# Performance work log

Measured on AMD Instinct MI355X. Metric: run time of the kernel, lower is better.

The kernel has to match this reference:

```python
import jax, jax.numpy as jnp
import numpy as np

EMBED_DIM = 1024
NUM_HEADS = 16
HEAD_DIM = EMBED_DIM // NUM_HEADS
WL_CHANNELS = 16
BATCH = 1
SEQ = 1024
KERR = 2.7e-18 * 1e6  # kerr_coefficient * 1e6 -> phase = KERR * |x|^2
SCALE = 1.0 / np.sqrt(HEAD_DIM)
W_INIT = 0.02


def setup_inputs() -> dict:
    key = jax.random.key(0)
    ks = jax.random.split(key, 7)
    x = jax.random.normal(ks[0], (BATCH, SEQ, EMBED_DIM), dtype=jnp.float32)
    Wq = jax.random.normal(ks[1], (EMBED_DIM, EMBED_DIM), dtype=jnp.float32) * W_INIT
    Wk = jax.random.normal(ks[2], (EMBED_DIM, EMBED_DIM), dtype=jnp.float32) * W_INIT
    Wv = jax.random.normal(ks[3], (EMBED_DIM, EMBED_DIM), dtype=jnp.float32) * W_INIT
    Wo = jax.random.normal(ks[4], (EMBED_DIM, EMBED_DIM), dtype=jnp.float32) * W_INIT
    bq = jnp.zeros((EMBED_DIM,), jnp.float32)
    bk = jnp.zeros((EMBED_DIM,), jnp.float32)
    bv = jnp.zeros((EMBED_DIM,), jnp.float32)
    bo = jnp.zeros((EMBED_DIM,), jnp.float32)
    phase_modulators = jax.random.normal(ks[5], (WL_CHANNELS, NUM_HEADS), dtype=jnp.float32)
    interference_weights = jnp.ones((WL_CHANNELS,), jnp.float32)
    return {"x": x, "Wq": Wq, "bq": bq, "Wk": Wk, "bk": bk, "Wv": Wv, "bv": bv,
            "Wo": Wo, "bo": bo, "phase_modulators": phase_modulators,
            "interference_weights": interference_weights}


def reference(x, Wq, bq, Wk, bk, Wv, bv, Wo, bo, phase_modulators, interference_weights):
    B, S, E = x.shape
    H, D = NUM_HEADS, HEAD_DIM

    def proj(W, b):
        # [B,S,E] -> [B,H,S,D]
        y = jnp.einsum('bse,ef->bsf', x, W) + b
        return y.reshape(B, S, H, D).transpose(0, 2, 1, 3)

    Q = proj(Wq, bq)
    K = proj(Wk, bk)
    V = proj(Wv, bv)

    # exp(1j*phase).real == cos(phase) for real phase
    cos_pm = jnp.cos(phase_modulators)  # [W, H]

    def wl_step(acc, wl):
        cpm, iw = wl  # cpm: [H], iw: scalar
        m = cpm[None, :, None, None]
        Qw = Q * m
        Kw = K * m
        scores = jnp.einsum('bhqd,bhkd->bhqk', Qw, Kw) * SCALE
        # Kerr nonlinearity: x * cos(KERR * x^2)
        scores = scores * jnp.cos(KERR * scores * scores)
        attn = jax.nn.softmax(scores, axis=-1)
        out = jnp.einsum('bhqk,bhkd->bhqd', attn, V)
        return acc + out * iw, None

    acc0 = jnp.zeros((B, H, S, D), x.dtype)
    acc, _ = jax.lax.scan(wl_step, acc0, (cos_pm, interference_weights))
    combined = acc / WL_CHANNELS  # mean over wavelength channels
    combined = combined.transpose(0, 2, 1, 3).reshape(B, S, E)
    return jnp.einsum('bse,ef->bsf', combined, Wo) + bo
```

## Files before the change

### kernel.cpp

```cpp
#include <hip/hip_runtime.h>
#include <hip/hip_fp16.h>
#include <math.h>

#define NH 16
#define NWL 16
#define NPOLY 10

typedef _Float16 half8 __attribute__((ext_vector_type(8)));
typedef _Float16 half4 __attribute__((ext_vector_type(4)));
typedef float f32x4 __attribute__((ext_vector_type(4)));

__global__ __launch_bounds__(256)
void cast_x_k(const float* __restrict__ X, _Float16* __restrict__ Xh)
{
    const int i = (blockIdx.x * 256 + threadIdx.x) * 8;
    float4 v0 = *(const float4*)&X[i];
    float4 v1 = *(const float4*)&X[i + 4];
    half8 o;
    o[0] = (_Float16)v0.x; o[1] = (_Float16)v0.y; o[2] = (_Float16)v0.z; o[3] = (_Float16)v0.w;
    o[4] = (_Float16)v1.x; o[5] = (_Float16)v1.y; o[6] = (_Float16)v1.z; o[7] = (_Float16)v1.w;
    *(half8*)&Xh[i] = o;
}

__global__ __launch_bounds__(256)
void castT_w(const float* __restrict__ W0, const float* __restrict__ W1,
             const float* __restrict__ W2, const float* __restrict__ W3,
             _Float16* __restrict__ WT)
{
    const float* W = W0;
    if (blockIdx.z == 1) W = W1;
    if (blockIdx.z == 2) W = W2;
    if (blockIdx.z == 3) W = W3;
    _Float16* out = WT + ((size_t)blockIdx.z << 20);

    __shared__ float Ts[64][65];
    const int t = threadIdx.x;
    const int ebase = blockIdx.y * 64;
    const int fbase = blockIdx.x * 64;

    {
        const int r0 = (t >> 4) * 4;
        const int c0 = (t & 15) * 4;
#pragma unroll
        for (int r = 0; r < 4; ++r) {
            float4 v = *(const float4*)&W[(size_t)(ebase + r0 + r) * 1024 + fbase + c0];
            Ts[r0 + r][c0 + 0] = v.x;
            Ts[r0 + r][c0 + 1] = v.y;
            Ts[r0 + r][c0 + 2] = v.z;
            Ts[r0 + r][c0 + 3] = v.w;
        }
    }
    __syncthreads();

    const int f = t >> 2;
    const int eseg = (t & 3) * 16;
    half8 lo, hi;
#pragma unroll
    for (int j = 0; j < 8; ++j) lo[j] = (_Float16)Ts[eseg + j][f];
#pragma unroll
    for (int j = 0; j < 8; ++j) hi[j] = (_Float16)Ts[eseg + 8 + j][f];
    *(half8*)&out[(size_t)(fbase + f) * 1024 + ebase + eseg]     = lo;
    *(half8*)&out[(size_t)(fbase + f) * 1024 + ebase + eseg + 8] = hi;
}

template<int MODE>
__global__ __launch_bounds__(256)
void gemm_mfma(const _Float16* __restrict__ A,
               const _Float16* __restrict__ BtBase,
               const float* __restrict__ B0, const float* __restrict__ B1,
               const float* __restrict__ B2,
               void* __restrict__ O0p, void* __restrict__ O1p, void* __restrict__ O2p)
{
    const int z = blockIdx.z;
    const _Float16* Bt = BtBase + ((size_t)z << 20);
    const float* bias = B0; void* Op = O0p;
    if (z == 1) { bias = B1; Op = O1p; }
    if (z == 2) { bias = B2; Op = O2p; }

    __shared__ _Float16 As[2][64][40];
    __shared__ _Float16 Bs[2][64][40];

    const int t = threadIdx.x;
    const int lane = t & 63;
    const int w = t >> 6;
    const int w_r = w >> 1;
    const int w_c = w & 1;
    const int sbase = blockIdx.y * 64;
    const int fbase = blockIdx.x * 64;

    const int srow = t >> 2;
    const int skseg = (t & 3) * 8;

    f32x4 acc[2][2];
#pragma unroll
    for (int m = 0; m < 2; ++m)
#pragma unroll
        for (int n = 0; n < 2; ++n) acc[m][n] = (f32x4){0.f, 0.f, 0.f, 0.f};

    const int lr = lane & 15;
    const int lk = (lane >> 4) * 8;

    {
        *(half8*)&As[0][srow][skseg] = *(const half8*)&A [(size_t)(sbase + srow) * 1024 + skseg];
        *(half8*)&Bs[0][srow][skseg] = *(const half8*)&Bt[(size_t)(fbase + srow) * 1024 + skseg];
    }
    __syncthreads();

    for (int tile = 0; tile < 32; ++tile) {
        const int cur = tile & 1;
        if (tile < 31) {
            const int kb = (tile + 1) * 32;
            half8 av = *(const half8*)&A [(size_t)(sbase + srow) * 1024 + kb + skseg];
            half8 bv = *(const half8*)&Bt[(size_t)(fbase + srow) * 1024 + kb + skseg];
            *(half8*)&As[cur ^ 1][srow][skseg] = av;
            *(half8*)&Bs[cur ^ 1][srow][skseg] = bv;
        }
        half8 a0 = *(const half8*)&As[cur][w_r * 32 + 0  + lr][lk];
        half8 a1 = *(const half8*)&As[cur][w_r * 32 + 16 + lr][lk];
        half8 b0 = *(const half8*)&Bs[cur][w_c * 32 + 0  + lr][lk];
        half8 b1 = *(const half8*)&Bs[cur][w_c * 32 + 16 + lr][lk];
        acc[0][0] = __builtin_amdgcn_mfma_f32_16x16x32_f16(a0, b0, acc[0][0], 0, 0, 0);
        acc[0][1] = __builtin_amdgcn_mfma_f32_16x16x32_f16(a0, b1, acc[0][1], 0, 0, 0);
        acc[1][0] = __builtin_amdgcn_mfma_f32_16x16x32_f16(a1, b0, acc[1][0], 0, 0, 0);
        acc[1][1] = __builtin_amdgcn_mfma_f32_16x16x32_f16(a1, b1, acc[1][1], 0, 0, 0);
        __syncthreads();
    }

#pragma unroll
    for (int m = 0; m < 2; ++m) {
        const int row0 = sbase + w_r * 32 + m * 16 + (lane >> 4) * 4;
#pragma unroll
        for (int n = 0; n < 2; ++n) {
            const int col = fbase + w_c * 32 + n * 16 + (lane & 15);
            const float bval = bias[col];
            if (MODE == 0) {
                float* O = (float*)Op;
#pragma unroll
                for (int r = 0; r < 4; ++r)
                    O[(size_t)(row0 + r) * 1024 + col] = acc[m][n][r] + bval;
            } else {
                _Float16* O = (_Float16*)Op;
                const int hh = col >> 6;
                const int d = col & 63;
                if (z == 2) {
                    half4 o;
#pragma unroll
                    for (int r = 0; r < 4; ++r) o[r] = (_Float16)(acc[m][n][r] + bval);
                    *(half4*)&O[((size_t)hh << 16) + (size_t)d * 1024 + row0] = o;
                } else {
#pragma unroll
                    for (int r = 0; r < 4; ++r)
                        O[((size_t)hh << 16) + (size_t)(row0 + r) * 64 + d] =
                            (_Float16)(acc[m][n][r] + bval);
                }
            }
        }
    }
}

__global__ __launch_bounds__(256, 4)
void attn_k(const _Float16* __restrict__ Qg, const _Float16* __restrict__ Kg,
            const _Float16* __restrict__ Vg, const float* __restrict__ pm,
            const float* __restrict__ iwp, _Float16* __restrict__ comb)
{
    const int wg  = blockIdx.x;
    const int xcd = wg & 7;
    const int idx = wg >> 3;
    const int h   = xcd * 2 + (idx >> 6);
    const int qt  = idx & 63;

    const int t = threadIdx.x;
    const int lane = t & 63;
    const int w = t >> 6;
    const int lr = lane & 15;
    const int lg = lane >> 4;

    __shared__ float Sred[4][16][68];
    __shared__ _Float16 Ps[4][16][72];
    __shared__ float sa[16], siw[16];
    __shared__ float gt[16][NPOLY + 1];

    if (t < 16) {
        float m = cosf(pm[t * NH + h]);
        sa[t] = m * m * 0.125f * 1.44269504f;
        siw[t] = iwp[t];
    }
    __syncthreads();

    float amin = sa[0], amax = sa[0];
#pragma unroll
    for (int i = 1; i < NWL; ++i) {
        amin = fminf(amin, sa[i]);
        amax = fmaxf(amax, sa[i]);
    }
    const float abar = 0.5f * (amin + amax);

    if (t < 16) {
        float g = (sa[t] - abar) * 0.69314718f;
        float p = 1.f;
        gt[t][0] = 1.f;
#pragma unroll
        for (int n = 1; n <= NPOLY; ++n) {
            p *= g / (float)n;
            gt[t][n] = p;
        }
    }

    const _Float16* Qrow = Qg + ((size_t)h << 16) + (size_t)(qt * 16 + lr) * 64;
    half8 q0 = *(const half8*)&Qrow[lg * 8];
    half8 q1 = *(const half8*)&Qrow[32 + lg * 8];
    __syncthreads();

    const _Float16* Kq = Kg + ((size_t)h << 16) + (size_t)w * 256 * 64;
    const _Float16* Vh = Vg + ((size_t)h << 16);

    float M[NPOLY + 1];
#pragma unroll
    for (int n = 0; n <= NPOLY; ++n) M[n] = 0.f;

    for (int ch = 0; ch < 4; ++ch) {
#pragma unroll
        for (int kf = 0; kf < 4; ++kf) {
            const _Float16* Kr = Kq + (size_t)(ch * 64 + kf * 16 + lr) * 64;
            half8 a0 = *(const half8*)&Kr[lg * 8];
            half8 a1 = *(const half8*)&Kr[32 + lg * 8];
            f32x4 s2 = (f32x4){0.f, 0.f, 0.f, 0.f};
            s2 = __builtin_amdgcn_mfma_f32_16x16x32_f16(a0, q0, s2, 0, 0, 0);
            s2 = __builtin_amdgcn_mfma_f32_16x16x32_f16(a1, q1, s2, 0, 0, 0);
#pragma unroll
            for (int r = 0; r < 4; ++r) {
                const float sv = s2[r];
                float e = exp2f(abar * sv);
                M[0] += e;
#pragma unroll
                for (int n = 1; n <= NPOLY; ++n) {
                    e *= sv;
                    M[n] += e;
                }
            }
        }
    }

#pragma unroll
    for (int off = 16; off < 64; off <<= 1)
#pragma unroll
        for (int n = 0; n <= NPOLY; ++n)
            M[n] += __shfl_xor(M[n], off);

    if (lg == 0) {
#pragma unroll
        for (int n = 0; n <= NPOLY; ++n) Sred[w][lr][n] = M[n];
    }
    __syncthreads();

#pragma unroll
    for (int n = 0; n <= NPOLY; ++n)
        M[n] = Sred[0][lr][n] + Sred[1][lr][n] + Sred[2][lr][n] + Sred[3][lr][n];

    float c[NPOLY + 1];
#pragma unroll
    for (int n = 0; n <= NPOLY; ++n) c[n] = 0.f;
#pragma unroll
    for (int i = 0; i < NWL; ++i) {
        float den = 0.f;
#pragma unroll
        for (int n = 0; n <= NPOLY; ++n) den = fmaf(gt[i][n], M[n], den);
        const float wgt = siw[i] / (den * 16.0f);
#pragma unroll
        for (int n = 0; n <= NPOLY; ++n) c[n] = fmaf(wgt, gt[i][n], c[n]);
    }
    __syncthreads();

    f32x4 oacc[4];
#pragma unroll
    for (int n = 0; n < 4; ++n) oacc[n] = (f32x4){0.f, 0.f, 0.f, 0.f};

    for (int ch = 0; ch < 4; ++ch) {
#pragma unroll
        for (int kf = 0; kf < 4; ++kf) {
            const _Float16* Kr = Kq + (size_t)(ch * 64 + kf * 16 + lr) * 64;
            half8 a0 = *(const half8*)&Kr[lg * 8];
            half8 a1 = *(const half8*)&Kr[32 + lg * 8];
            f32x4 s2 = (f32x4){0.f, 0.f, 0.f, 0.f};
            s2 = __builtin_amdgcn_mfma_f32_16x16x32_f16(a0, q0, s2, 0, 0, 0);
            s2 = __builtin_amdgcn_mfma_f32_16x16x32_f16(a1, q1, s2, 0, 0, 0);
            half4 ph;
#pragma unroll
            for (int r = 0; r < 4; ++r) {
                const float sv = s2[r];
                const float e = exp2f(abar * sv);
                float poly = c[NPOLY];
#pragma unroll
                for (int n = NPOLY - 1; n >= 0; --n)
                    poly = fmaf(poly, sv, c[n]);
                ph[r] = (_Float16)(e * poly);
            }
            *(half4*)&Ps[w][lr][kf * 16 + lg * 4] = ph;
        }
        half8 pa0 = *(const half8*)&Ps[w][lr][lg * 8];
        half8 pa1 = *(const half8*)&Ps[w][lr][32 + lg * 8];
        const int kcol = w * 256 + ch * 64;
#pragma unroll
        for (int n = 0; n < 4; ++n) {
            const _Float16* Vr = Vh + (size_t)(n * 16 + lr) * 1024 + kcol;
            half8 vb0 = *(const half8*)&Vr[lg * 8];
            half8 vb1 = *(const half8*)&Vr[32 + lg * 8];
            oacc[n] = __builtin_amdgcn_mfma_f32_16x16x32_f16(pa0, vb0, oacc[n], 0, 0, 0);
            oacc[n] = __builtin_amdgcn_mfma_f32_16x16x32_f16(pa1, vb1, oacc[n], 0, 0, 0);
        }
    }

#pragma unroll
    for (int n = 0; n < 4; ++n)
#pragma unroll
        for (int r = 0; r < 4; ++r)
            Sred[w][lg * 4 + r][n * 16 + lr] = oacc[n][r];
    __syncthreads();

    {
        const int q = t >> 4;
        const int d0 = (t & 15) * 4;
        f32x4 s0 = *(const f32x4*)&Sred[0][q][d0];
        f32x4 s1 = *(const f32x4*)&Sred[1][q][d0];
        f32x4 s2v = *(const f32x4*)&Sred[2][q][d0];
        f32x4 s3 = *(const f32x4*)&Sred[3][q][d0];
        f32x4 sum = s0 + s1 + s2v + s3;
        half4 o;
#pragma unroll
        for (int r = 0; r < 4; ++r) o[r] = (_Float16)sum[r];
        *(half4*)&comb[(size_t)(qt * 16 + q) * 1024 + h * 64 + d0] = o;
    }
}

extern "C" void kernel_launch(void* const* d_in, const int* in_sizes, int n_in,
                              void* d_out, int out_size, void* d_ws, size_t ws_size,
                              hipStream_t stream)
{
    const float* x  = (const float*)d_in[0];
    const float* Wq = (const float*)d_in[1];
    const float* bq = (const float*)d_in[2];
    const float* Wk = (const float*)d_in[3];
    const float* bk = (const float*)d_in[4];
    const float* Wv = (const float*)d_in[5];
    const float* bv = (const float*)d_in[6];
    const float* Wo = (const float*)d_in[7];
    const float* bo = (const float*)d_in[8];
    const float* pm = (const float*)d_in[9];
    const float* iw = (const float*)d_in[10];
    float* out = (float*)d_out;

    _Float16* Xh = (_Float16*)d_ws;
    _Float16* WT = Xh + (1u << 20);
    _Float16* Qh = WT + (4u << 20);
    _Float16* Kh = Qh + (1u << 20);
    _Float16* Vt = Kh + (1u << 20);
    _Float16* comb = Xh;

    dim3 blk(256);
    cast_x_k<<<dim3(512), blk, 0, stream>>>(x, Xh);
    castT_w<<<dim3(16, 16, 4), blk, 0, stream>>>(Wq, Wk, Wv, Wo, WT);
    gemm_mfma<1><<<dim3(16, 16, 3), blk, 0, stream>>>(Xh, WT, bq, bk, bv, Qh, Kh, Vt);
    attn_k<<<dim3(1024), blk, 0, stream>>>(Qh, Kh, Vt, pm, iw, comb);
    gemm_mfma<0><<<dim3(16, 16, 1), blk, 0, stream>>>(
        comb, WT + (3u << 20), bo, bo, bo, out, out, out);
}
```

Measured before the change: 100.8 us.

## Split attention keys across eight waves and cut the moment polynomial order

The attention kernel now runs 512 threads per block, so each of eight waves handles 128 keys instead of 256. The cross-wave reductions change to match: per-wave moment sums are gathered through a dedicated shared buffer, and output partials are reduced in two halves. The truncated series that folds the 16 wavelength channels into one polynomial per query drops from 10 to 5 terms, which roughly halves the per-score moment and polynomial arithmetic. The shorter series risks accuracy when the channel scale factors are spread widely, and the larger block raises register pressure per block.

```diff
diff --git a/kernel.cpp b/kernel.cpp
--- a/kernel.cpp
+++ b/kernel.cpp
@@ -4,10 +4,11 @@
 
 #define NH 16
 #define NWL 16
-#define NPOLY 10
+#define NPOLY 5
 
 typedef _Float16 half8 __attribute__((ext_vector_type(8)));
 typedef _Float16 half4 __attribute__((ext_vector_type(4)));
+typedef _Float16 half2v __attribute__((ext_vector_type(2)));
 typedef float f32x4 __attribute__((ext_vector_type(4)));
 
 __global__ __launch_bounds__(256)
@@ -158,7 +159,7 @@
     }
 }
 
-__global__ __launch_bounds__(256, 4)
+__global__ __launch_bounds__(512, 8)
 void attn_k(const _Float16* __restrict__ Qg, const _Float16* __restrict__ Kg,
             const _Float16* __restrict__ Vg, const float* __restrict__ pm,
             const float* __restrict__ iwp, _Float16* __restrict__ comb)
@@ -175,8 +176,9 @@
     const int lr = lane & 15;
     const int lg = lane >> 4;
 
-    __shared__ float Sred[4][16][68];
-    __shared__ _Float16 Ps[4][16][72];
+    __shared__ float Red[4][16][68];
+    __shared__ float Mom[8][16][8];
+    __shared__ _Float16 Ps[8][16][68];
     __shared__ float sa[16], siw[16];
     __shared__ float gt[16][NPOLY + 1];
 
@@ -209,34 +211,31 @@
     const _Float16* Qrow = Qg + ((size_t)h << 16) + (size_t)(qt * 16 + lr) * 64;
     half8 q0 = *(const half8*)&Qrow[lg * 8];
     half8 q1 = *(const half8*)&Qrow[32 + lg * 8];
-    __syncthreads();
-
-    const _Float16* Kq = Kg + ((size_t)h << 16) + (size_t)w * 256 * 64;
+
+    const _Float16* Kq = Kg + ((size_t)h << 16) + (size_t)(w * 128) * 64;
     const _Float16* Vh = Vg + ((size_t)h << 16);
 
     float M[NPOLY + 1];
 #pragma unroll
     for (int n = 0; n <= NPOLY; ++n) M[n] = 0.f;
 
-    for (int ch = 0; ch < 4; ++ch) {
-#pragma unroll
-        for (int kf = 0; kf < 4; ++kf) {
-            const _Float16* Kr = Kq + (size_t)(ch * 64 + kf * 16 + lr) * 64;
-            half8 a0 = *(const half8*)&Kr[lg * 8];
-            half8 a1 = *(const half8*)&Kr[32 + lg * 8];
-            f32x4 s2 = (f32x4){0.f, 0.f, 0.f, 0.f};
-            s2 = __builtin_amdgcn_mfma_f32_16x16x32_f16(a0, q0, s2, 0, 0, 0);
-            s2 = __builtin_amdgcn_mfma_f32_16x16x32_f16(a1, q1, s2, 0, 0, 0);
-#pragma unroll
-            for (int r = 0; r < 4; ++r) {
-                const float sv = s2[r];
-                float e = exp2f(abar * sv);
-                M[0] += e;
-#pragma unroll
-                for (int n = 1; n <= NPOLY; ++n) {
-                    e *= sv;
-                    M[n] += e;
-                }
+#pragma unroll
+    for (int kf = 0; kf < 8; ++kf) {
+        const _Float16* Kr = Kq + (size_t)(kf * 16 + lr) * 64;
+        half8 a0 = *(const half8*)&Kr[lg * 8];
+        half8 a1 = *(const half8*)&Kr[32 + lg * 8];
+        f32x4 s2 = (f32x4){0.f, 0.f, 0.f, 0.f};
+        s2 = __builtin_amdgcn_mfma_f32_16x16x32_f16(a0, q0, s2, 0, 0, 0);
+        s2 = __builtin_amdgcn_mfma_f32_16x16x32_f16(a1, q1, s2, 0, 0, 0);
+#pragma unroll
+        for (int r = 0; r < 4; ++r) {
+            const float sv = s2[r];
+            float e = exp2f(abar * sv);
+            M[0] += e;
+#pragma unroll
+            for (int n = 1; n <= NPOLY; ++n) {
+                e *= sv;
+                M[n] += e;
             }
         }
     }
@@ -249,13 +248,17 @@
 
     if (lg == 0) {
 #pragma unroll
-        for (int n = 0; n <= NPOLY; ++n) Sred[w][lr][n] = M[n];
-    }
-    __syncthreads();
-
-#pragma unroll
-    for (int n = 0; n <= NPOLY; ++n)
-        M[n] = Sred[0][lr][n] + Sred[1][lr][n] + Sred[2][lr][n] + Sred[3][lr][n];
+        for (int n = 0; n <= NPOLY; ++n) Mom[w][lr][n] = M[n];
+    }
+    __syncthreads();
+
+#pragma unroll
+    for (int n = 0; n <= NPOLY; ++n) {
+        float s = 0.f;
+#pragma unroll
+        for (int ww = 0; ww < 8; ++ww) s += Mom[ww][lr][n];
+        M[n] = s;
+    }
 
     float c[NPOLY + 1];
 #pragma unroll
@@ -269,13 +272,13 @@
 #pragma unroll
         for (int n = 0; n <= NPOLY; ++n) c[n] = fmaf(wgt, gt[i][n], c[n]);
     }
-    __syncthreads();
 
     f32x4 oacc[4];
 #pragma unroll
     for (int n = 0; n < 4; ++n) oacc[n] = (f32x4){0.f, 0.f, 0.f, 0.f};
 
-    for (int ch = 0; ch < 4; ++ch) {
+#pragma unroll
+    for (int ch = 0; ch < 2; ++ch) {
 #pragma unroll
         for (int kf = 0; kf < 4; ++kf) {
             const _Float16* Kr = Kq + (size_t)(ch * 64 + kf * 16 + lr) * 64;
@@ -299,7 +302,7 @@
         }
         half8 pa0 = *(const half8*)&Ps[w][lr][lg * 8];
         half8 pa1 = *(const half8*)&Ps[w][lr][32 + lg * 8];
-        const int kcol = w * 256 + ch * 64;
+        const int kcol = w * 128 + ch * 64;
 #pragma unroll
         for (int n = 0; n < 4; ++n) {
             const _Float16* Vr = Vh + (size_t)(n * 16 + lr) * 1024 + kcol;
@@ -310,25 +313,32 @@
         }
     }
 
-#pragma unroll
-    for (int n = 0; n < 4; ++n)
-#pragma unroll
-        for (int r = 0; r < 4; ++r)
-            Sred[w][lg * 4 + r][n * 16 + lr] = oacc[n][r];
+    if (w >= 4) {
+#pragma unroll
+        for (int n = 0; n < 4; ++n)
+#pragma unroll
+            for (int r = 0; r < 4; ++r)
+                Red[w - 4][lg * 4 + r][n * 16 + lr] = oacc[n][r];
+    }
+    __syncthreads();
+    if (w < 4) {
+#pragma unroll
+        for (int n = 0; n < 4; ++n)
+#pragma unroll
+            for (int r = 0; r < 4; ++r)
+                Red[w][lg * 4 + r][n * 16 + lr] += oacc[n][r];
+    }
     __syncthreads();
 
     {
-        const int q = t >> 4;
-        const int d0 = (t & 15) * 4;
-        f32x4 s0 = *(const f32x4*)&Sred[0][q][d0];
-        f32x4 s1 = *(const f32x4*)&Sred[1][q][d0];
-        f32x4 s2v = *(const f32x4*)&Sred[2][q][d0];
-        f32x4 s3 = *(const f32x4*)&Sred[3][q][d0];
-        f32x4 sum = s0 + s1 + s2v + s3;
-        half4 o;
-#pragma unroll
-        for (int r = 0; r < 4; ++r) o[r] = (_Float16)sum[r];
-        *(half4*)&comb[(size_t)(qt * 16 + q) * 1024 + h * 64 + d0] = o;
+        const int q = t >> 5;
+        const int d0 = (t & 31) * 2;
+        float s0 = Red[0][q][d0] + Red[1][q][d0] + Red[2][q][d0] + Red[3][q][d0];
+        float s1 = Red[0][q][d0 + 1] + Red[1][q][d0 + 1] + Red[2][q][d0 + 1] + Red[3][q][d0 + 1];
+        half2v o;
+        o[0] = (_Float16)s0;
+        o[1] = (_Float16)s1;
+        *(half2v*)&comb[(size_t)(qt * 16 + q) * 1024 + h * 64 + d0] = o;
     }
 }
 
@@ -360,7 +370,7 @@
     cast_x_k<<<dim3(512), blk, 0, stream>>>(x, Xh);
     castT_w<<<dim3(16, 16, 4), blk, 0, stream>>>(Wq, Wk, Wv, Wo, WT);
     gemm_mfma<1><<<dim3(16, 16, 3), blk, 0, stream>>>(Xh, WT, bq, bk, bv, Qh, Kh, Vt);
-    attn_k<<<dim3(1024), blk, 0, stream>>>(Qh, Kh, Vt, pm, iw, comb);
+    attn_k<<<dim3(1024), dim3(512), 0, stream>>>(Qh, Kh, Vt, pm, iw, comb);
     gemm_mfma<0><<<dim3(16, 16, 1), blk, 0, stream>>>(
         comb, WT + (3u << 20), bo, bo, bo, out, out, out);
 }
```

New measurement: 117.5 us. +16.6%, slower.

## Single-pass attention via four moment-weighted PV accumulators with cubic Taylor expansion

Applied to the files above, without the earlier changes.

Replaces the two-pass scheme (moments pass, then a recompute of QK^T and a polynomial-weighted PV pass) with a single pass. It computes four weighted probability matrices e*s^m (m=0..3), multiplies each by V with MFMA, and combines them afterwards with per-row coefficients. The Taylor expansion of the per-wavelength scale is cut from 10 terms to 3. This removes the second QK^T and exp computation but quadruples the PV MFMAs and accumulator registers, and the lower-order expansion risks accuracy.

```diff
diff --git a/kernel.cpp b/kernel.cpp
--- a/kernel.cpp
+++ b/kernel.cpp
@@ -4,7 +4,6 @@
 
 #define NH 16
 #define NWL 16
-#define NPOLY 10
 
 typedef _Float16 half8 __attribute__((ext_vector_type(8)));
 typedef _Float16 half4 __attribute__((ext_vector_type(4)));
@@ -175,10 +174,13 @@
     const int lr = lane & 15;
     const int lg = lane >> 4;
 
-    __shared__ float Sred[4][16][68];
-    __shared__ _Float16 Ps[4][16][72];
+    __shared__ union {
+        _Float16 Ps[4][4][16][68];
+        struct { float Mom[4][16][4]; float Red[4][16][68]; } E;
+    } U;
     __shared__ float sa[16], siw[16];
-    __shared__ float gt[16][NPOLY + 1];
+    __shared__ float gt[16][4];
+    __shared__ float Ctab[16][4];
 
     if (t < 16) {
         float m = cosf(pm[t * NH + h]);
@@ -197,26 +199,25 @@
 
     if (t < 16) {
         float g = (sa[t] - abar) * 0.69314718f;
-        float p = 1.f;
         gt[t][0] = 1.f;
-#pragma unroll
-        for (int n = 1; n <= NPOLY; ++n) {
-            p *= g / (float)n;
-            gt[t][n] = p;
-        }
+        gt[t][1] = g;
+        gt[t][2] = g * g * 0.5f;
+        gt[t][3] = g * g * g * (1.f / 6.f);
     }
 
     const _Float16* Qrow = Qg + ((size_t)h << 16) + (size_t)(qt * 16 + lr) * 64;
     half8 q0 = *(const half8*)&Qrow[lg * 8];
     half8 q1 = *(const half8*)&Qrow[32 + lg * 8];
-    __syncthreads();
-
-    const _Float16* Kq = Kg + ((size_t)h << 16) + (size_t)w * 256 * 64;
+
+    const _Float16* Kq = Kg + ((size_t)h << 16) + (size_t)(w * 256) * 64;
     const _Float16* Vh = Vg + ((size_t)h << 16);
 
-    float M[NPOLY + 1];
-#pragma unroll
-    for (int n = 0; n <= NPOLY; ++n) M[n] = 0.f;
+    float M0 = 0.f, M1 = 0.f, M2 = 0.f, M3 = 0.f;
+    f32x4 macc[4][4];
+#pragma unroll
+    for (int m = 0; m < 4; ++m)
+#pragma unroll
+        for (int n = 0; n < 4; ++n) macc[m][n] = (f32x4){0.f, 0.f, 0.f, 0.f};
 
     for (int ch = 0; ch < 4; ++ch) {
 #pragma unroll
@@ -227,103 +228,103 @@
             f32x4 s2 = (f32x4){0.f, 0.f, 0.f, 0.f};
             s2 = __builtin_amdgcn_mfma_f32_16x16x32_f16(a0, q0, s2, 0, 0, 0);
             s2 = __builtin_amdgcn_mfma_f32_16x16x32_f16(a1, q1, s2, 0, 0, 0);
+            half4 p0, p1, p2, p3;
 #pragma unroll
             for (int r = 0; r < 4; ++r) {
                 const float sv = s2[r];
-                float e = exp2f(abar * sv);
-                M[0] += e;
-#pragma unroll
-                for (int n = 1; n <= NPOLY; ++n) {
-                    e *= sv;
-                    M[n] += e;
-                }
+                const float e   = exp2f(abar * sv);
+                const float es  = e * sv;
+                const float tt  = sv * sv;
+                const float et  = e * tt;
+                const float est = es * tt;
+                M0 += e; M1 += es; M2 += et; M3 += est;
+                p0[r] = (_Float16)e;
+                p1[r] = (_Float16)es;
+                p2[r] = (_Float16)et;
+                p3[r] = (_Float16)est;
             }
-        }
-    }
-
-#pragma unroll
-    for (int off = 16; off < 64; off <<= 1)
-#pragma unroll
-        for (int n = 0; n <= NPOLY; ++n)
-            M[n] += __shfl_xor(M[n], off);
-
+            const int kl = kf * 16 + lg * 4;
+            *(half4*)&U.Ps[w][0][lr][kl] = p0;
+            *(half4*)&U.Ps[w][1][lr][kl] = p1;
+            *(half4*)&U.Ps[w][2][lr][kl] = p2;
+            *(half4*)&U.Ps[w][3][lr][kl] = p3;
+        }
+        const int kcol = w * 256 + ch * 64;
+#pragma unroll
+        for (int m = 0; m < 4; ++m) {
+            half8 pa0 = *(const half8*)&U.Ps[w][m][lr][lg * 8];
+            half8 pa1 = *(const half8*)&U.Ps[w][m][lr][32 + lg * 8];
+#pragma unroll
+            for (int n = 0; n < 4; ++n) {
+                const _Float16* Vr = Vh + (size_t)(n * 16 + lr) * 1024 + kcol;
+                half8 vb0 = *(const half8*)&Vr[lg * 8];
+                half8 vb1 = *(const half8*)&Vr[32 + lg * 8];
+                macc[m][n] = __builtin_amdgcn_mfma_f32_16x16x32_f16(pa0, vb0, macc[m][n], 0, 0, 0);
+                macc[m][n] = __builtin_amdgcn_mfma_f32_16x16x32_f16(pa1, vb1, macc[m][n], 0, 0, 0);
+            }
+        }
+    }
+    __syncthreads();
+
+#pragma unroll
+    for (int off = 16; off < 64; off <<= 1) {
+        M0 += __shfl_xor(M0, off);
+        M1 += __shfl_xor(M1, off);
+        M2 += __shfl_xor(M2, off);
+        M3 += __shfl_xor(M3, off);
+    }
     if (lg == 0) {
-#pragma unroll
-        for (int n = 0; n <= NPOLY; ++n) Sred[w][lr][n] = M[n];
-    }
-    __syncthreads();
-
-#pragma unroll
-    for (int n = 0; n <= NPOLY; ++n)
-        M[n] = Sred[0][lr][n] + Sred[1][lr][n] + Sred[2][lr][n] + Sred[3][lr][n];
-
-    float c[NPOLY + 1];
-#pragma unroll
-    for (int n = 0; n <= NPOLY; ++n) c[n] = 0.f;
+        U.E.Mom[w][lr][0] = M0;
+        U.E.Mom[w][lr][1] = M1;
+        U.E.Mom[w][lr][2] = M2;
+        U.E.Mom[w][lr][3] = M3;
+    }
+    __syncthreads();
+
+    float Mf[4];
+#pragma unroll
+    for (int m = 0; m < 4; ++m)
+        Mf[m] = U.E.Mom[0][lr][m] + U.E.Mom[1][lr][m] + U.E.Mom[2][lr][m] + U.E.Mom[3][lr][m];
+
+    float c0 = 0.f, c1 = 0.f, c2 = 0.f, c3 = 0.f;
 #pragma unroll
     for (int i = 0; i < NWL; ++i) {
-        float den = 0.f;
-#pragma unroll
-        for (int n = 0; n <= NPOLY; ++n) den = fmaf(gt[i][n], M[n], den);
+        float den = gt[i][0] * Mf[0];
+        den = fmaf(gt[i][1], Mf[1], den);
+        den = fmaf(gt[i][2], Mf[2], den);
+        den = fmaf(gt[i][3], Mf[3], den);
         const float wgt = siw[i] / (den * 16.0f);
-#pragma unroll
-        for (int n = 0; n <= NPOLY; ++n) c[n] = fmaf(wgt, gt[i][n], c[n]);
-    }
-    __syncthreads();
-
-    f32x4 oacc[4];
-#pragma unroll
-    for (int n = 0; n < 4; ++n) oacc[n] = (f32x4){0.f, 0.f, 0.f, 0.f};
-
-    for (int ch = 0; ch < 4; ++ch) {
-#pragma unroll
-        for (int kf = 0; kf < 4; ++kf) {
-            const _Float16* Kr = Kq + (size_t)(ch * 64 + kf * 16 + lr) * 64;
-            half8 a0 = *(const half8*)&Kr[lg * 8];
-            half8 a1 = *(const half8*)&Kr[32 + lg * 8];
-            f32x4 s2 = (f32x4){0.f, 0.f, 0.f, 0.f};
-            s2 = __builtin_amdgcn_mfma_f32_16x16x32_f16(a0, q0, s2, 0, 0, 0);
-            s2 = __builtin_amdgcn_mfma_f32_16x16x32_f16(a1, q1, s2, 0, 0, 0);
-            half4 ph;
-#pragma unroll
-            for (int r = 0; r < 4; ++r) {
-                const float sv = s2[r];
-                const float e = exp2f(abar * sv);
-                float poly = c[NPOLY];
-#pragma unroll
-                for (int n = NPOLY - 1; n >= 0; --n)
-                    poly = fmaf(poly, sv, c[n]);
-                ph[r] = (_Float16)(e * poly);
-            }
-            *(half4*)&Ps[w][lr][kf * 16 + lg * 4] = ph;
-        }
-        half8 pa0 = *(const half8*)&Ps[w][lr][lg * 8];
-        half8 pa1 = *(const half8*)&Ps[w][lr][32 + lg * 8];
-        const int kcol = w * 256 + ch * 64;
-#pragma unroll
-        for (int n = 0; n < 4; ++n) {
-            const _Float16* Vr = Vh + (size_t)(n * 16 + lr) * 1024 + kcol;
-            half8 vb0 = *(const half8*)&Vr[lg * 8];
-            half8 vb1 = *(const half8*)&Vr[32 + lg * 8];
-            oacc[n] = __builtin_amdgcn_mfma_f32_16x16x32_f16(pa0, vb0, oacc[n], 0, 0, 0);
-            oacc[n] = __builtin_amdgcn_mfma_f32_16x16x32_f16(pa1, vb1, oacc[n], 0, 0, 0);
-        }
-    }
-
-#pragma unroll
-    for (int n = 0; n < 4; ++n)
-#pragma unroll
-        for (int r = 0; r < 4; ++r)
-            Sred[w][lg * 4 + r][n * 16 + lr] = oacc[n][r];
+        c0 = fmaf(wgt, gt[i][0], c0);
+        c1 = fmaf(wgt, gt[i][1], c1);
+        c2 = fmaf(wgt, gt[i][2], c2);
+        c3 = fmaf(wgt, gt[i][3], c3);
+    }
+    if (t < 16) {
+        Ctab[t][0] = c0; Ctab[t][1] = c1; Ctab[t][2] = c2; Ctab[t][3] = c3;
+    }
+    __syncthreads();
+
+#pragma unroll
+    for (int n = 0; n < 4; ++n) {
+#pragma unroll
+        for (int r = 0; r < 4; ++r) {
+            const int q = lg * 4 + r;
+            float o = Ctab[q][0] * macc[0][n][r];
+            o = fmaf(Ctab[q][1], macc[1][n][r], o);
+            o = fmaf(Ctab[q][2], macc[2][n][r], o);
+            o = fmaf(Ctab[q][3], macc[3][n][r], o);
+            U.E.Red[w][q][n * 16 + lr] = o;
+        }
+    }
     __syncthreads();
 
     {
         const int q = t >> 4;
         const int d0 = (t & 15) * 4;
-        f32x4 s0 = *(const f32x4*)&Sred[0][q][d0];
-        f32x4 s1 = *(const f32x4*)&Sred[1][q][d0];
-        f32x4 s2v = *(const f32x4*)&Sred[2][q][d0];
-        f32x4 s3 = *(const f32x4*)&Sred[3][q][d0];
+        f32x4 s0 = *(const f32x4*)&U.E.Red[0][q][d0];
+        f32x4 s1 = *(const f32x4*)&U.E.Red[1][q][d0];
+        f32x4 s2v = *(const f32x4*)&U.E.Red[2][q][d0];
+        f32x4 s3 = *(const f32x4*)&U.E.Red[3][q][d0];
         f32x4 sum = s0 + s1 + s2v + s3;
         half4 o;
 #pragma unroll
```

Result: slower. 127.0 us (+26.0%).

## Split moment and PV passes into separate split-K kernels with cubic expansion

Applied to the files above, without the earlier changes.

The single attention kernel is replaced by three kernels. A moment kernel computes per-row exponential moments over quarter-key chunks. A PV kernel combines those moments into polynomial coefficients and accumulates P·V over half of the keys. A reduction kernel sums the two halves into the combined layout. The Taylor expansion over wavelength channels is cut from degree 10 to degree 3, which removes most per-score ALU work and raises grid size for better CU occupancy, at the cost of extra launches, partial-result traffic and a coarser approximation that depends on the spread of the phase modulators.

```diff
diff --git a/kernel.cpp b/kernel.cpp
--- a/kernel.cpp
+++ b/kernel.cpp
@@ -4,7 +4,6 @@
 
 #define NH 16
 #define NWL 16
-#define NPOLY 10
 
 typedef _Float16 half8 __attribute__((ext_vector_type(8)));
 typedef _Float16 half4 __attribute__((ext_vector_type(4)));
@@ -159,15 +158,16 @@
 }
 
 __global__ __launch_bounds__(256, 4)
-void attn_k(const _Float16* __restrict__ Qg, const _Float16* __restrict__ Kg,
-            const _Float16* __restrict__ Vg, const float* __restrict__ pm,
-            const float* __restrict__ iwp, _Float16* __restrict__ comb)
+void mom_k(const _Float16* __restrict__ Qg, const _Float16* __restrict__ Kg,
+           const float* __restrict__ pm, float* __restrict__ Mpart)
 {
     const int wg  = blockIdx.x;
     const int xcd = wg & 7;
     const int idx = wg >> 3;
-    const int h   = xcd * 2 + (idx >> 6);
-    const int qt  = idx & 63;
+    const int h   = xcd * 2 + (idx >> 8);
+    const int rem = idx & 255;
+    const int qt  = rem >> 2;
+    const int kq  = rem & 3;
 
     const int t = threadIdx.x;
     const int lane = t & 63;
@@ -175,10 +175,102 @@
     const int lr = lane & 15;
     const int lg = lane >> 4;
 
-    __shared__ float Sred[4][16][68];
-    __shared__ _Float16 Ps[4][16][72];
+    __shared__ float sa[16];
+    __shared__ float MomL[4][16][4];
+
+    if (t < 16) {
+        float m = cosf(pm[t * NH + h]);
+        sa[t] = m * m * 0.125f * 1.44269504f;
+    }
+    __syncthreads();
+
+    float amin = sa[0], amax = sa[0];
+#pragma unroll
+    for (int i = 1; i < NWL; ++i) {
+        amin = fminf(amin, sa[i]);
+        amax = fmaxf(amax, sa[i]);
+    }
+    const float abar = 0.5f * (amin + amax);
+
+    const _Float16* Qrow = Qg + ((size_t)h << 16) + (size_t)(qt * 16 + lr) * 64;
+    half8 q0 = *(const half8*)&Qrow[lg * 8];
+    half8 q1 = *(const half8*)&Qrow[32 + lg * 8];
+
+    const _Float16* Kbase = Kg + ((size_t)h << 16) + (size_t)(kq * 256 + w * 64) * 64;
+
+    float M0 = 0.f, M1 = 0.f, M2 = 0.f, M3 = 0.f;
+#pragma unroll
+    for (int kf = 0; kf < 4; ++kf) {
+        const _Float16* Kr = Kbase + (size_t)(kf * 16 + lr) * 64;
+        half8 a0 = *(const half8*)&Kr[lg * 8];
+        half8 a1 = *(const half8*)&Kr[32 + lg * 8];
+        f32x4 s2 = (f32x4){0.f, 0.f, 0.f, 0.f};
+        s2 = __builtin_amdgcn_mfma_f32_16x16x32_f16(a0, q0, s2, 0, 0, 0);
+        s2 = __builtin_amdgcn_mfma_f32_16x16x32_f16(a1, q1, s2, 0, 0, 0);
+#pragma unroll
+        for (int r = 0; r < 4; ++r) {
+            const float sv = s2[r];
+            const float e  = exp2f(abar * sv);
+            const float es = e * sv;
+            const float t2 = sv * sv;
+            M0 += e;
+            M1 += es;
+            M2 += e * t2;
+            M3 += es * t2;
+        }
+    }
+
+#pragma unroll
+    for (int off = 16; off < 64; off <<= 1) {
+        M0 += __shfl_xor(M0, off);
+        M1 += __shfl_xor(M1, off);
+        M2 += __shfl_xor(M2, off);
+        M3 += __shfl_xor(M3, off);
+    }
+    if (lg == 0) {
+        MomL[w][lr][0] = M0;
+        MomL[w][lr][1] = M1;
+        MomL[w][lr][2] = M2;
+        MomL[w][lr][3] = M3;
+    }
+    __syncthreads();
+
+    if (t < 64) {
+        const int row = t >> 2;
+        const int m = t & 3;
+        const float s = MomL[0][row][m] + MomL[1][row][m]
+                      + MomL[2][row][m] + MomL[3][row][m];
+        Mpart[(((size_t)(h * 64 + qt) * 4 + kq) * 16 + row) * 4 + m] = s;
+    }
+}
+
+__global__ __launch_bounds__(256, 4)
+void pvm_k(const _Float16* __restrict__ Qg, const _Float16* __restrict__ Kg,
+           const _Float16* __restrict__ Vg, const float* __restrict__ pm,
+           const float* __restrict__ iwp, const float* __restrict__ Mpart,
+           _Float16* __restrict__ Opart)
+{
+    const int wg  = blockIdx.x;
+    const int xcd = wg & 7;
+    const int idx = wg >> 3;
+    const int h   = xcd * 2 + (idx >> 7);
+    const int rem = idx & 127;
+    const int qt  = rem >> 1;
+    const int kh  = rem & 1;
+
+    const int t = threadIdx.x;
+    const int lane = t & 63;
+    const int w = t >> 6;
+    const int lr = lane & 15;
+    const int lg = lane >> 4;
+
+    __shared__ union {
+        _Float16 Ps[4][16][68];
+        float Red[4][16][68];
+    } U;
     __shared__ float sa[16], siw[16];
-    __shared__ float gt[16][NPOLY + 1];
+    __shared__ float gt[16][4];
+    __shared__ float Ctab[16][4];
 
     if (t < 16) {
         float m = cosf(pm[t * NH + h]);
@@ -197,88 +289,60 @@
 
     if (t < 16) {
         float g = (sa[t] - abar) * 0.69314718f;
-        float p = 1.f;
         gt[t][0] = 1.f;
-#pragma unroll
-        for (int n = 1; n <= NPOLY; ++n) {
-            p *= g / (float)n;
-            gt[t][n] = p;
-        }
-    }
+        gt[t][1] = g;
+        gt[t][2] = g * g * 0.5f;
+        gt[t][3] = g * g * g * (1.f / 6.f);
+    }
+    __syncthreads();
+
+    if (t < 16) {
+        const float* mp = &Mpart[(size_t)(h * 64 + qt) * 256 + t * 4];
+        float Mf0 = 0.f, Mf1 = 0.f, Mf2 = 0.f, Mf3 = 0.f;
+#pragma unroll
+        for (int k2 = 0; k2 < 4; ++k2) {
+            Mf0 += mp[k2 * 64 + 0];
+            Mf1 += mp[k2 * 64 + 1];
+            Mf2 += mp[k2 * 64 + 2];
+            Mf3 += mp[k2 * 64 + 3];
+        }
+        float c0 = 0.f, c1 = 0.f, c2 = 0.f, c3 = 0.f;
+#pragma unroll
+        for (int i = 0; i < NWL; ++i) {
+            float den = gt[i][0] * Mf0;
+            den = fmaf(gt[i][1], Mf1, den);
+            den = fmaf(gt[i][2], Mf2, den);
+            den = fmaf(gt[i][3], Mf3, den);
+            const float wgt = siw[i] / (den * 16.0f);
+            c0 = fmaf(wgt, gt[i][0], c0);
+            c1 = fmaf(wgt, gt[i][1], c1);
+            c2 = fmaf(wgt, gt[i][2], c2);
+            c3 = fmaf(wgt, gt[i][3], c3);
+        }
+        Ctab[t][0] = c0; Ctab[t][1] = c1; Ctab[t][2] = c2; Ctab[t][3] = c3;
+    }
+    __syncthreads();
+
+    const float c0 = Ctab[lr][0], c1 = Ctab[lr][1];
+    const float c2 = Ctab[lr][2], c3 = Ctab[lr][3];
 
     const _Float16* Qrow = Qg + ((size_t)h << 16) + (size_t)(qt * 16 + lr) * 64;
     half8 q0 = *(const half8*)&Qrow[lg * 8];
     half8 q1 = *(const half8*)&Qrow[32 + lg * 8];
-    __syncthreads();
-
-    const _Float16* Kq = Kg + ((size_t)h << 16) + (size_t)w * 256 * 64;
+
+    const int k0 = kh * 512 + w * 128;
+    const _Float16* Kbase = Kg + ((size_t)h << 16) + (size_t)k0 * 64;
     const _Float16* Vh = Vg + ((size_t)h << 16);
 
-    float M[NPOLY + 1];
-#pragma unroll
-    for (int n = 0; n <= NPOLY; ++n) M[n] = 0.f;
-
-    for (int ch = 0; ch < 4; ++ch) {
+    f32x4 oacc[4];
+#pragma unroll
+    for (int n = 0; n < 4; ++n) oacc[n] = (f32x4){0.f, 0.f, 0.f, 0.f};
+
+#pragma unroll
+    for (int ch = 0; ch < 2; ++ch) {
 #pragma unroll
         for (int kf = 0; kf < 4; ++kf) {
-            const _Float16* Kr = Kq + (size_t)(ch * 64 + kf * 16 + lr) * 64;
-            half8 a0 = *(const half8*)&Kr[lg * 8];
-            half8 a1 = *(const half8*)&Kr[32 + lg * 8];
-            f32x4 s2 = (f32x4){0.f, 0.f, 0.f, 0.f};
-            s2 = __builtin_amdgcn_mfma_f32_16x16x32_f16(a0, q0, s2, 0, 0, 0);
-            s2 = __builtin_amdgcn_mfma_f32_16x16x32_f16(a1, q1, s2, 0, 0, 0);
-#pragma unroll
-            for (int r = 0; r < 4; ++r) {
-                const float sv = s2[r];
-                float e = exp2f(abar * sv);
-                M[0] += e;
-#pragma unroll
-                for (int n = 1; n <= NPOLY; ++n) {
-                    e *= sv;
-                    M[n] += e;
-                }
-            }
-        }
-    }
-
-#pragma unroll
-    for (int off = 16; off < 64; off <<= 1)
-#pragma unroll
-        for (int n = 0; n <= NPOLY; ++n)
-            M[n] += __shfl_xor(M[n], off);
-
-    if (lg == 0) {
-#pragma unroll
-        for (int n = 0; n <= NPOLY; ++n) Sred[w][lr][n] = M[n];
-    }
-    __syncthreads();
-
-#pragma unroll
-    for (int n = 0; n <= NPOLY; ++n)
-        M[n] = Sred[0][lr][n] + Sred[1][lr][n] + Sred[2][lr][n] + Sred[3][lr][n];
-
-    float c[NPOLY + 1];
-#pragma unroll
-    for (int n = 0; n <= NPOLY; ++n) c[n] = 0.f;
-#pragma unroll
-    for (int i = 0; i < NWL; ++i) {
-        float den = 0.f;
-#pragma unroll
-        for (int n = 0; n <= NPOLY; ++n) den = fmaf(gt[i][n], M[n], den);
-        const float wgt = siw[i] / (den * 16.0f);
-#pragma unroll
-        for (int n = 0; n <= NPOLY; ++n) c[n] = fmaf(wgt, gt[i][n], c[n]);
-    }
-    __syncthreads();
-
-    f32x4 oacc[4];
-#pragma unroll
-    for (int n = 0; n < 4; ++n) oacc[n] = (f32x4){0.f, 0.f, 0.f, 0.f};
-
-    for (int ch = 0; ch < 4; ++ch) {
-#pragma unroll
-        for (int kf = 0; kf < 4; ++kf) {
-            const _Float16* Kr = Kq + (size_t)(ch * 64 + kf * 16 + lr) * 64;
+            const _Float16* Kr = Kbase + (size_t)(ch * 64 + kf * 16 + lr) * 64;
             half8 a0 = *(const half8*)&Kr[lg * 8];
             half8 a1 = *(const half8*)&Kr[32 + lg * 8];
             f32x4 s2 = (f32x4){0.f, 0.f, 0.f, 0.f};
@@ -289,17 +353,16 @@
             for (int r = 0; r < 4; ++r) {
                 const float sv = s2[r];
                 const float e = exp2f(abar * sv);
-                float poly = c[NPOLY];
-#pragma unroll
-                for (int n = NPOLY - 1; n >= 0; --n)
-                    poly = fmaf(poly, sv, c[n]);
+                float poly = fmaf(c3, sv, c2);
+                poly = fmaf(poly, sv, c1);
+                poly = fmaf(poly, sv, c0);
                 ph[r] = (_Float16)(e * poly);
             }
-            *(half4*)&Ps[w][lr][kf * 16 + lg * 4] = ph;
-        }
-        half8 pa0 = *(const half8*)&Ps[w][lr][lg * 8];
-        half8 pa1 = *(const half8*)&Ps[w][lr][32 + lg * 8];
-        const int kcol = w * 256 + ch * 64;
+            *(half4*)&U.Ps[w][lr][kf * 16 + lg * 4] = ph;
+        }
+        half8 pa0 = *(const half8*)&U.Ps[w][lr][lg * 8];
+        half8 pa1 = *(const half8*)&U.Ps[w][lr][32 + lg * 8];
+        const int kcol = k0 + ch * 64;
 #pragma unroll
         for (int n = 0; n < 4; ++n) {
             const _Float16* Vr = Vh + (size_t)(n * 16 + lr) * 1024 + kcol;
@@ -309,27 +372,48 @@
             oacc[n] = __builtin_amdgcn_mfma_f32_16x16x32_f16(pa1, vb1, oacc[n], 0, 0, 0);
         }
     }
+    __syncthreads();
 
 #pragma unroll
     for (int n = 0; n < 4; ++n)
 #pragma unroll
         for (int r = 0; r < 4; ++r)
-            Sred[w][lg * 4 + r][n * 16 + lr] = oacc[n][r];
+            U.Red[w][lg * 4 + r][n * 16 + lr] = oacc[n][r];
     __syncthreads();
 
     {
         const int q = t >> 4;
         const int d0 = (t & 15) * 4;
-        f32x4 s0 = *(const f32x4*)&Sred[0][q][d0];
-        f32x4 s1 = *(const f32x4*)&Sred[1][q][d0];
-        f32x4 s2v = *(const f32x4*)&Sred[2][q][d0];
-        f32x4 s3 = *(const f32x4*)&Sred[3][q][d0];
+        f32x4 s0 = *(const f32x4*)&U.Red[0][q][d0];
+        f32x4 s1 = *(const f32x4*)&U.Red[1][q][d0];
+        f32x4 s2v = *(const f32x4*)&U.Red[2][q][d0];
+        f32x4 s3 = *(const f32x4*)&U.Red[3][q][d0];
         f32x4 sum = s0 + s1 + s2v + s3;
         half4 o;
 #pragma unroll
-        for (int r = 0; r < 4; ++r) o[r] = (_Float16)sum[r];
-        *(half4*)&comb[(size_t)(qt * 16 + q) * 1024 + h * 64 + d0] = o;
-    }
+        for (int j = 0; j < 4; ++j) o[j] = (_Float16)sum[j];
+        _Float16* dst = &Opart[(((size_t)kh * 16 + h) * 64 + qt) * 1024 + q * 64 + d0];
+        *(half4*)dst = o;
+    }
+}
+
+__global__ __launch_bounds__(256)
+void ored_k(const _Float16* __restrict__ Opart, _Float16* __restrict__ comb)
+{
+    const int gid = blockIdx.x * 256 + threadIdx.x;
+    const int h  = gid >> 14;
+    const int r  = gid & 16383;
+    const int qt = r >> 8;
+    const int q  = (r >> 4) & 15;
+    const int d0 = (r & 15) * 4;
+    const size_t base = (((size_t)h * 64 + qt) * 16 + q) * 64 + d0;
+    const size_t plane = (size_t)16 * 64 * 16 * 64;
+    half4 a = *(const half4*)&Opart[base];
+    half4 b = *(const half4*)&Opart[base + plane];
+    half4 o;
+#pragma unroll
+    for (int j = 0; j < 4; ++j) o[j] = (_Float16)((float)a[j] + (float)b[j]);
+    *(half4*)&comb[(size_t)(qt * 16 + q) * 1024 + h * 64 + d0] = o;
 }
 
 extern "C" void kernel_launch(void* const* d_in, const int* in_sizes, int n_in,
@@ -354,13 +438,17 @@
     _Float16* Qh = WT + (4u << 20);
     _Float16* Kh = Qh + (1u << 20);
     _Float16* Vt = Kh + (1u << 20);
+    _Float16* Opart = Vt + (1u << 20);
+    float* Mpart = (float*)WT;
     _Float16* comb = Xh;
 
     dim3 blk(256);
     cast_x_k<<<dim3(512), blk, 0, stream>>>(x, Xh);
     castT_w<<<dim3(16, 16, 4), blk, 0, stream>>>(Wq, Wk, Wv, Wo, WT);
     gemm_mfma<1><<<dim3(16, 16, 3), blk, 0, stream>>>(Xh, WT, bq, bk, bv, Qh, Kh, Vt);
-    attn_k<<<dim3(1024), blk, 0, stream>>>(Qh, Kh, Vt, pm, iw, comb);
+    mom_k<<<dim3(4096), blk, 0, stream>>>(Qh, Kh, pm, Mpart);
+    pvm_k<<<dim3(2048), blk, 0, stream>>>(Qh, Kh, Vt, pm, iw, Mpart, Opart);
+    ored_k<<<dim3(1024), blk, 0, stream>>>(Opart, comb);
     gemm_mfma<0><<<dim3(16, 16, 1), blk, 0, stream>>>(
         comb, WT + (3u << 20), bo, bo, bo, out, out, out);
 }
```

New measurement: 112.1 us. 11.2% more time.
